# Kernel optimization log

Measured on AMD Instinct MI355X. Metric: run time of the kernel, lower is better.

The kernel has to match this reference:

```python
import jax, jax.numpy as jnp
import numpy as np

UNITS = 50257
CUTOFF = [2000, 10000, UNITS]   # cutoff + [units], as in __init__
D = 1024
FACTOR = 4
N_CLUST = len(CUTOFF) - 1       # 2 tail clusters
HEAD_OUT = CUTOFF[0] + N_CLUST  # 2002 = head classes + one logit per cluster


def _tail_dims():
    dims = []
    for i in range(N_CLUST):
        dim = D / FACTOR ** (i + 1)
        dims.append(max(1, round(dim / 8)) * 8)
    return dims  # [256, 64]


def setup_inputs() -> dict:
    key = jax.random.key(0)
    ks = jax.random.split(key, 16)
    B, T = 2, 1024
    x = jax.random.normal(ks[0], (B, T, D), jnp.float32)
    targets = jax.random.randint(ks[1], (B, T), 0, UNITS)
    inp = {
        'x': x,
        'targets': targets,
        # head: Dense(D -> HEAD_OUT), use_bias=False (glorot-ish scaling)
        'head_kernel': jax.random.normal(ks[2], (D, HEAD_OUT), jnp.float32) / np.float32(np.sqrt(D)),
    }
    for i, dim in enumerate(_tail_dims()):
        out = CUTOFF[i + 1] - CUTOFF[i]
        inp[f'proj_kernel_{i}'] = jax.random.normal(ks[3 + 4 * i], (D, dim), jnp.float32) / np.float32(np.sqrt(D))
        inp[f'proj_bias_{i}'] = jnp.zeros((dim,), jnp.float32)
        inp[f'scale_kernel_{i}'] = jax.random.normal(ks[4 + 4 * i], (dim, out), jnp.float32) / np.float32(np.sqrt(dim))
        inp[f'scale_bias_{i}'] = jnp.zeros((out,), jnp.float32)
    return inp


def reference(x, targets, head_kernel,
              proj_kernel_0, proj_bias_0, scale_kernel_0, scale_bias_0,
              proj_kernel_1, proj_bias_1, scale_kernel_1, scale_bias_1):
    # Head: root logits over [head classes | cluster logits]
    root_logits = jnp.einsum('btd,dh->bth', x, head_kernel)          # [B,T,HEAD_OUT]
    root_logprobs = jax.nn.log_softmax(root_logits, axis=-1)
    parts = [root_logprobs[..., :CUTOFF[0]]]                          # head class logprobs
    tails = [(proj_kernel_0, proj_bias_0, scale_kernel_0, scale_bias_0),
             (proj_kernel_1, proj_bias_1, scale_kernel_1, scale_bias_1)]
    for i, (pk, pb, sk, sb) in enumerate(tails):
        h = jnp.einsum('btd,dk->btk', x, pk) + pb                     # low-rank projection
        logits = jnp.einsum('btk,kv->btv', h, sk) + sb                # cluster vocab slice
        clust_lp = root_logprobs[..., CUTOFF[0] + i:CUTOFF[0] + i + 1]
        parts.append(jax.nn.log_softmax(logits, axis=-1) + clust_lp)  # P(w) = P(cluster)*P(w|cluster)
    logprobs = jnp.concatenate(parts, axis=-1)                        # [B,T,UNITS]
    return jnp.exp(logprobs)
```

## Files before the change

### kernel.cpp

```cpp
#include <hip/hip_runtime.h>
#include <cstdint>
#include <cstddef>

#define ROWS    2048
#define DIM     1024
#define VOCAB   50257
#define CUT0    2000
#define CUT1    10000
#define PROJ_LD 320
#define LGTC_LD 10016

typedef __attribute__((ext_vector_type(8))) _Float16 f16x8;
typedef __attribute__((ext_vector_type(4))) float    f32x4;

__device__ __forceinline__ void gload_lds16(const void* g, void* l) {
    __builtin_amdgcn_global_load_lds(
        (const __attribute__((address_space(1))) void*)g,
        (__attribute__((address_space(3))) void*)l, 16, 0, 0);
}

__device__ __forceinline__ int swz8(int i, int n) {
    return (i & 7) * (n >> 3) + (i >> 3);
}

__device__ __forceinline__ void transpose_tile(
    const float* __restrict__ src, _Float16* __restrict__ dst,
    int K, int N, int local, int ntiles, float* tile)
{
    const int t  = threadIdx.x;
    const int bn = local % ntiles, bk = local / ntiles;
    const int tx = t & 31, ty = t >> 5;
    const int n0 = bn * 32, k0 = bk * 32;
#pragma unroll
    for (int i = 0; i < 4; ++i) {
        int kk = ty + i * 8;
        int n  = n0 + tx;
        tile[kk * 33 + tx] = (n < N) ? src[(size_t)(k0 + kk) * N + n] : 0.f;
    }
    __syncthreads();
#pragma unroll
    for (int i = 0; i < 4; ++i) {
        int nn = ty + i * 8;
        int r  = n0 + nn;
        dst[(size_t)r * K + k0 + tx] = (_Float16)tile[tx * 33 + nn];
    }
}

__global__ __launch_bounds__(256)
void k1_convert(const float* __restrict__ x, const float* __restrict__ head,
                const float* __restrict__ pk0, const float* __restrict__ pk1,
                _Float16* __restrict__ A, _Float16* __restrict__ headT,
                _Float16* __restrict__ pkT, float* __restrict__ S)
{
    __shared__ float tile[32 * 33];
    const int bid = blockIdx.x, t = threadIdx.x;

    if (bid >= 4480) {
        int i = (bid - 4480) * 256 + t;
        ((float4*)S)[i] = make_float4(0.f, 0.f, 0.f, 0.f);
        return;
    }
    if (bid < 2048) {
        int fid = bid * 256 + t;
        float4 v = ((const float4*)x)[fid];
        union { _Float16 h[4]; ushort4 u; } cv;
        cv.h[0] = (_Float16)v.x; cv.h[1] = (_Float16)v.y;
        cv.h[2] = (_Float16)v.z; cv.h[3] = (_Float16)v.w;
        ((ushort4*)A)[fid] = cv.u;
        return;
    }
    if (bid < 4096)
        transpose_tile(head, headT, 1024, 2002, bid - 2048, 64, tile);
    else if (bid < 4352)
        transpose_tile(pk0, pkT, 1024, 256, bid - 4096, 8, tile);
    else
        transpose_tile(pk1, pkT + 256 * 1024, 1024, 64, bid - 4352, 4, tile);
}

template<int MODE, int BM>
__device__ __forceinline__ void gemm_body(
    _Float16* As, _Float16* Bs,
    const _Float16* __restrict__ A, int lda,
    const _Float16* __restrict__ B, int K,
    int bx, int by, int Nvalid,
    const float* __restrict__ bias,
    const float* __restrict__ pb0, const float* __restrict__ pb1,
    _Float16* __restrict__ lgtC, float* __restrict__ root2,
    float* __restrict__ S, float* __restrict__ outF,
    _Float16* __restrict__ h)
{
    const int t    = threadIdx.x;
    const int lane = t & 63;
    const int w    = t >> 6;
    const int wr   = w >> 1, wc = w & 1;
    const int q    = lane >> 4, cl = lane & 15;
    const int row0blk = by * BM;
    const int col0blk = bx * 128;
    constexpr int MR = BM / 32;

    f32x4 acc[MR][4];
#pragma unroll
    for (int m = 0; m < MR; ++m)
#pragma unroll
        for (int n = 0; n < 4; ++n)
            acc[m][n] = (f32x4){0.f, 0.f, 0.f, 0.f};

    for (int k0 = 0; k0 < K; k0 += 64) {
        __syncthreads();
#pragma unroll
        for (int iss = 0; iss < MR; ++iss) {
            int ci  = iss * 256 + w * 64 + lane;
            int row = ci >> 3;
            int ch  = (ci & 7) ^ (row & 7);
            gload_lds16(A + (size_t)(row0blk + row) * lda + k0 + ch * 8,
                        As + (size_t)(iss * 256 + w * 64) * 8);
        }
#pragma unroll
        for (int iss = 0; iss < 4; ++iss) {
            int ci  = iss * 256 + w * 64 + lane;
            int row = ci >> 3;
            int ch  = (ci & 7) ^ (row & 7);
            gload_lds16(B + (size_t)(col0blk + row) * K + k0 + ch * 8,
                        Bs + (size_t)(iss * 256 + w * 64) * 8);
        }
        __syncthreads();

#pragma unroll
        for (int kk = 0; kk < 2; ++kk) {
            f16x8 a[MR], b[4];
#pragma unroll
            for (int m = 0; m < MR; ++m) {
                int row = wr * (BM / 2) + m * 16 + cl;
                int ch  = (kk * 4 + q) ^ (row & 7);
                a[m] = *(const f16x8*)(As + row * 64 + ch * 8);
            }
#pragma unroll
            for (int n = 0; n < 4; ++n) {
                int row = wc * 64 + n * 16 + cl;
                int ch  = (kk * 4 + q) ^ (row & 7);
                b[n] = *(const f16x8*)(Bs + row * 64 + ch * 8);
            }
#pragma unroll
            for (int m = 0; m < MR; ++m)
#pragma unroll
                for (int n = 0; n < 4; ++n)
                    acc[m][n] = __builtin_amdgcn_mfma_f32_16x16x32_f16(
                        a[m], b[n], acc[m][n], 0, 0, 0);
        }
    }
    __syncthreads();

    if (MODE == 3) {
#pragma unroll
        for (int m = 0; m < MR; ++m)
#pragma unroll
            for (int n = 0; n < 4; ++n) {
                int colseg = col0blk + wc * 64 + n * 16 + cl;
                if (colseg < PROJ_LD) {
                    float bv = (colseg < 256) ? pb0[colseg] : pb1[colseg - 256];
#pragma unroll
                    for (int j = 0; j < 4; ++j) {
                        int rg = row0blk + wr * (BM / 2) + m * 16 + q * 4 + j;
                        h[(size_t)rg * PROJ_LD + colseg] =
                            (_Float16)(acc[m][n][j] + bv);
                    }
                }
            }
        return;
    }

    float bn4[4];
#pragma unroll
    for (int n = 0; n < 4; ++n) {
        int colseg = col0blk + wc * 64 + n * 16 + cl;
        bn4[n] = (MODE != 0 && colseg < Nvalid) ? bias[colseg] : 0.f;
    }

    if (MODE == 4) {
#pragma unroll
        for (int m = 0; m < MR; ++m)
#pragma unroll
            for (int j = 0; j < 4; ++j) {
                int rg = row0blk + wr * (BM / 2) + m * 16 + q * 4 + j;
                float4 S4 = ((const float4*)S)[rg];
                float scl = __expf(root2[rg * 2 + 1]) / (S4.z * S4.x);
                size_t rb = (size_t)rg * VOCAB + CUT1;
#pragma unroll
                for (int n = 0; n < 4; ++n) {
                    int c = col0blk + wc * 64 + n * 16 + cl;
                    if (c < Nvalid)
                        outF[rb + c] = __expf(acc[m][n][j] + bn4[n]) * scl;
                }
            }
        return;
    }

    float* sred = (float*)As;
#pragma unroll
    for (int m = 0; m < MR; ++m)
#pragma unroll
        for (int j = 0; j < 4; ++j) {
            int rloc = wr * (BM / 2) + m * 16 + q * 4 + j;
            int rg   = row0blk + rloc;
            float sm = 0.f;
#pragma unroll
            for (int n = 0; n < 4; ++n) {
                int c = col0blk + wc * 64 + n * 16 + cl;
                float v = acc[m][n][j] + bn4[n];
                bool ok = c < Nvalid;
                if (MODE == 0 && ok) {
                    if (c < CUT0)
                        lgtC[(size_t)rg * LGTC_LD + c] = (_Float16)v;
                    else
                        root2[rg * 2 + (c - CUT0)] = v;
                }
                if (MODE == 1 && ok)
                    lgtC[(size_t)rg * LGTC_LD + CUT0 + c] = (_Float16)v;
                sm += ok ? __expf(v) : 0.f;
            }
#pragma unroll
            for (int d = 1; d < 16; d <<= 1)
                sm += __shfl_xor(sm, d);
            if (cl == 0) sred[wc * BM + rloc] = sm;
        }
    __syncthreads();
    if (t < BM) {
        const int sidx = (MODE == 0) ? 0 : (MODE == 1 ? 1 : 2);
        atomicAdd(&S[(row0blk + t) * 4 + sidx], sred[t] + sred[BM + t]);
    }
}

__global__ __launch_bounds__(256)
void k2_projroot(const _Float16* __restrict__ A, const _Float16* __restrict__ pkT,
                 const _Float16* __restrict__ headT,
                 const float* __restrict__ sk0, const float* __restrict__ sk1,
                 const float* __restrict__ pb0, const float* __restrict__ pb1,
                 _Float16* __restrict__ h, _Float16* __restrict__ lgtC,
                 _Float16* __restrict__ sk0T, _Float16* __restrict__ sk1T,
                 float* __restrict__ root2, float* __restrict__ S)
{
    __shared__ _Float16 As[128 * 64];
    __shared__ _Float16 Bs[128 * 64];
    const int bid = blockIdx.x;
    if (bid < 512) {
        int i = swz8(bid, 512);
        gemm_body<0, 64>(As, Bs, A, DIM, headT, 1024, i % 16, i / 16, 2002,
                         nullptr, nullptr, nullptr, lgtC, root2, S, nullptr,
                         nullptr);
    } else if (bid < 560) {
        int i = swz8(bid - 512, 48);
        gemm_body<3, 128>(As, Bs, A, DIM, pkT, 1024, i % 3, i / 3, PROJ_LD,
                          nullptr, pb0, pb1, nullptr, nullptr, nullptr,
                          nullptr, h);
    } else if (bid < 2576) {
        transpose_tile(sk0, sk0T, 256, 8000, bid - 560, 252, (float*)As);
    } else {
        transpose_tile(sk1, sk1T, 64, 40257, bid - 2576, 1260, (float*)As);
    }
}

__global__ __launch_bounds__(256)
void k3_scales(const _Float16* __restrict__ h, const _Float16* __restrict__ sk0T,
               const _Float16* __restrict__ sk1T,
               const float* __restrict__ sb0, const float* __restrict__ sb1,
               _Float16* __restrict__ lgtC, float* __restrict__ S)
{
    __shared__ _Float16 As[128 * 64];
    __shared__ _Float16 Bs[128 * 64];
    const int bid = blockIdx.x;
    if (bid < 1008) {
        int i = swz8(bid, 1008);
        gemm_body<1, 128>(As, Bs, h, PROJ_LD, sk0T, 256, i % 63, i / 63, 8000,
                          sb0, nullptr, nullptr, lgtC, nullptr, S, nullptr,
                          nullptr);
    } else {
        int i = swz8(bid - 1008, 5040);
        gemm_body<2, 128>(As, Bs, h + 256, PROJ_LD, sk1T, 64, i % 315, i / 315,
                          40257, sb1, nullptr, nullptr, nullptr, nullptr, S,
                          nullptr, nullptr);
    }
}

__global__ __launch_bounds__(256)
void k4_megafin(const _Float16* __restrict__ h, const _Float16* __restrict__ sk1T,
                const float* __restrict__ sb1, const _Float16* __restrict__ lgtC,
                const float* __restrict__ root2, const float* __restrict__ S,
                float* __restrict__ outF)
{
    __shared__ _Float16 As[128 * 64];
    __shared__ _Float16 Bs[128 * 64];
    const int bid = blockIdx.x;
    if (bid < 5040) {
        int i = swz8(bid, 5040);
        gemm_body<4, 128>(As, Bs, h + 256, PROJ_LD, sk1T, 64, i % 315, i / 315,
                          40257, sb1, nullptr, nullptr, nullptr,
                          (float*)root2, (float*)S, outF, nullptr);
        return;
    }
    const int r = bid - 5040;
    float4 S4 = ((const float4*)S)[r];
    float inv_r = 1.f / S4.x;
    float sc0   = __expf(root2[r * 2 + 0]) / (S4.y * S4.x);
    const _Float16* lrow = lgtC + (size_t)r * LGTC_LD;
    float* orow = outF + (size_t)r * VOCAB;
    for (int i8 = threadIdx.x; i8 < LGTC_LD / 8; i8 += 256) {
        uint4 raw = *(const uint4*)(lrow + i8 * 8);
        union { uint32_t u; _Float16 hh[2]; } pp[4];
        pp[0].u = raw.x; pp[1].u = raw.y; pp[2].u = raw.z; pp[3].u = raw.w;
        int c0 = i8 * 8;
#pragma unroll
        for (int k = 0; k < 4; ++k)
#pragma unroll
            for (int j = 0; j < 2; ++j) {
                int c = c0 + k * 2 + j;
                if (c < CUT1) {
                    float sc = (c < CUT0) ? inv_r : sc0;
                    orow[c] = __expf((float)pp[k].hh[j]) * sc;
                }
            }
    }
}

extern "C" void kernel_launch(void* const* d_in, const int* in_sizes, int n_in,
                              void* d_out, int out_size, void* d_ws, size_t ws_size,
                              hipStream_t stream)
{
    (void)in_sizes; (void)n_in; (void)out_size; (void)ws_size;

    const float* x    = (const float*)d_in[0];
    const float* head = (const float*)d_in[2];
    const float* pk0  = (const float*)d_in[3];
    const float* pb0  = (const float*)d_in[4];
    const float* sk0  = (const float*)d_in[5];
    const float* sb0  = (const float*)d_in[6];
    const float* pk1  = (const float*)d_in[7];
    const float* pb1  = (const float*)d_in[8];
    const float* sk1  = (const float*)d_in[9];
    const float* sb1  = (const float*)d_in[10];

    float* out = (float*)d_out;
    char*  ws  = (char*)d_ws;

    _Float16* lgtC  = (_Float16*)(ws);
    _Float16* A     = (_Float16*)(ws + 41025536);
    _Float16* headT = (_Float16*)(ws + 45219840);
    _Float16* pkT   = (_Float16*)(ws + 49414144);
    _Float16* sk0T  = (_Float16*)(ws + 50200576);
    _Float16* sk1T  = (_Float16*)(ws + 54329344);
    _Float16* h     = (_Float16*)(ws + 59490304);
    float*    root2 = (float*)(ws + 60801024);
    float*    S     = (float*)(ws + 60817408);

    const dim3 blk(256);

    k1_convert<<<dim3(4488), blk, 0, stream>>>(x, head, pk0, pk1,
                                               A, headT, pkT, S);
    k2_projroot<<<dim3(5096), blk, 0, stream>>>(A, pkT, headT, sk0, sk1,
                                                pb0, pb1, h, lgtC, sk0T, sk1T,
                                                root2, S);
    k3_scales<<<dim3(6048), blk, 0, stream>>>(h, sk0T, sk1T, sb0, sb1, lgtC, S);
    k4_megafin<<<dim3(7088), blk, 0, stream>>>(h, sk1T, sb1, lgtC, root2, S, out);
}
```

Baseline: 266.6 us.

## Replace LDS-staged GEMM with direct-register MFMA for small-K tail scale GEMMs

```diff
diff --git a/kernel.cpp b/kernel.cpp
--- a/kernel.cpp
+++ b/kernel.cpp
@@ -83,11 +83,9 @@
     const _Float16* __restrict__ A, int lda,
     const _Float16* __restrict__ B, int K,
     int bx, int by, int Nvalid,
-    const float* __restrict__ bias,
     const float* __restrict__ pb0, const float* __restrict__ pb1,
     _Float16* __restrict__ lgtC, float* __restrict__ root2,
-    float* __restrict__ S, float* __restrict__ outF,
-    _Float16* __restrict__ h)
+    float* __restrict__ S, _Float16* __restrict__ h)
 {
     const int t    = threadIdx.x;
     const int lane = t & 63;
@@ -169,19 +167,100 @@
         return;
     }
 
+    float* sred = (float*)As;
+#pragma unroll
+    for (int m = 0; m < MR; ++m)
+#pragma unroll
+        for (int j = 0; j < 4; ++j) {
+            int rloc = wr * (BM / 2) + m * 16 + q * 4 + j;
+            int rg   = row0blk + rloc;
+            float sm = 0.f;
+#pragma unroll
+            for (int n = 0; n < 4; ++n) {
+                int c = col0blk + wc * 64 + n * 16 + cl;
+                float v = acc[m][n][j];
+                bool ok = c < Nvalid;
+                if (ok) {
+                    if (c < CUT0)
+                        lgtC[(size_t)rg * LGTC_LD + c] = (_Float16)v;
+                    else
+                        root2[rg * 2 + (c - CUT0)] = v;
+                }
+                sm += ok ? __expf(v) : 0.f;
+            }
+#pragma unroll
+            for (int d = 1; d < 16; d <<= 1)
+                sm += __shfl_xor(sm, d);
+            if (cl == 0) sred[wc * BM + rloc] = sm;
+        }
+    __syncthreads();
+    if (t < BM)
+        atomicAdd(&S[(row0blk + t) * 4 + 0], sred[t] + sred[BM + t]);
+}
+
+template<int MODE, int KK>
+__device__ __forceinline__ void gemm_direct(
+    const _Float16* __restrict__ A, int lda,
+    const _Float16* __restrict__ B,
+    int bx, int by, int Nvalid,
+    const float* __restrict__ bias,
+    _Float16* __restrict__ lgtC, const float* __restrict__ root2,
+    float* __restrict__ S, float* __restrict__ outF)
+{
+    __shared__ float sred[256];
+    const int t    = threadIdx.x;
+    const int lane = t & 63;
+    const int w    = t >> 6;
+    const int wr   = w >> 1, wc = w & 1;
+    const int q    = lane >> 4, cl = lane & 15;
+    const int row0blk = by * 128;
+    const int col0blk = bx * 128;
+
+    f32x4 acc[4][4];
+#pragma unroll
+    for (int m = 0; m < 4; ++m)
+#pragma unroll
+        for (int n = 0; n < 4; ++n)
+            acc[m][n] = (f32x4){0.f, 0.f, 0.f, 0.f};
+
+    const _Float16* ap[4];
+    const _Float16* bp[4];
+#pragma unroll
+    for (int m = 0; m < 4; ++m)
+        ap[m] = A + (size_t)(row0blk + wr * 64 + m * 16 + cl) * lda + q * 8;
+#pragma unroll
+    for (int n = 0; n < 4; ++n)
+        bp[n] = B + (size_t)(col0blk + wc * 64 + n * 16 + cl) * KK + q * 8;
+
+#pragma unroll
+    for (int ks = 0; ks < KK / 32; ++ks) {
+        const int ko = ks * 32;
+        f16x8 a[4], b[4];
+#pragma unroll
+        for (int m = 0; m < 4; ++m) a[m] = *(const f16x8*)(ap[m] + ko);
+#pragma unroll
+        for (int n = 0; n < 4; ++n) b[n] = *(const f16x8*)(bp[n] + ko);
+#pragma unroll
+        for (int m = 0; m < 4; ++m)
+#pragma unroll
+            for (int n = 0; n < 4; ++n)
+                acc[m][n] = __builtin_amdgcn_mfma_f32_16x16x32_f16(
+                    a[m], b[n], acc[m][n], 0, 0, 0);
+    }
+
     float bn4[4];
 #pragma unroll
     for (int n = 0; n < 4; ++n) {
         int colseg = col0blk + wc * 64 + n * 16 + cl;
-        bn4[n] = (MODE != 0 && colseg < Nvalid) ? bias[colseg] : 0.f;
+        bn4[n] = (colseg < Nvalid) ? bias[colseg] : 0.f;
     }
 
     if (MODE == 4) {
 #pragma unroll
-        for (int m = 0; m < MR; ++m)
+        for (int m = 0; m < 4; ++m)
 #pragma unroll
             for (int j = 0; j < 4; ++j) {
-                int rg = row0blk + wr * (BM / 2) + m * 16 + q * 4 + j;
+                int rg = row0blk + wr * 64 + m * 16 + q * 4 + j;
                 float4 S4 = ((const float4*)S)[rg];
                 float scl = __expf(root2[rg * 2 + 1]) / (S4.z * S4.x);
                 size_t rb = (size_t)rg * VOCAB + CUT1;
@@ -195,12 +274,11 @@
         return;
     }
 
-    float* sred = (float*)As;
-#pragma unroll
-    for (int m = 0; m < MR; ++m)
+#pragma unroll
+    for (int m = 0; m < 4; ++m)
 #pragma unroll
         for (int j = 0; j < 4; ++j) {
-            int rloc = wr * (BM / 2) + m * 16 + q * 4 + j;
+            int rloc = wr * 64 + m * 16 + q * 4 + j;
             int rg   = row0blk + rloc;
             float sm = 0.f;
 #pragma unroll
@@ -208,12 +286,6 @@
                 int c = col0blk + wc * 64 + n * 16 + cl;
                 float v = acc[m][n][j] + bn4[n];
                 bool ok = c < Nvalid;
-                if (MODE == 0 && ok) {
-                    if (c < CUT0)
-                        lgtC[(size_t)rg * LGTC_LD + c] = (_Float16)v;
-                    else
-                        root2[rg * 2 + (c - CUT0)] = v;
-                }
                 if (MODE == 1 && ok)
                     lgtC[(size_t)rg * LGTC_LD + CUT0 + c] = (_Float16)v;
                 sm += ok ? __expf(v) : 0.f;
@@ -221,12 +293,12 @@
 #pragma unroll
             for (int d = 1; d < 16; d <<= 1)
                 sm += __shfl_xor(sm, d);
-            if (cl == 0) sred[wc * BM + rloc] = sm;
+            if (cl == 0) sred[wc * 128 + rloc] = sm;
         }
     __syncthreads();
-    if (t < BM) {
-        const int sidx = (MODE == 0) ? 0 : (MODE == 1 ? 1 : 2);
-        atomicAdd(&S[(row0blk + t) * 4 + sidx], sred[t] + sred[BM + t]);
+    if (t < 128) {
+        const int sidx = (MODE == 1) ? 1 : 2;
+        atomicAdd(&S[(row0blk + t) * 4 + sidx], sred[t] + sred[128 + t]);
     }
 }
 
@@ -245,13 +317,11 @@
     if (bid < 512) {
         int i = swz8(bid, 512);
         gemm_body<0, 64>(As, Bs, A, DIM, headT, 1024, i % 16, i / 16, 2002,
-                         nullptr, nullptr, nullptr, lgtC, root2, S, nullptr,
-                         nullptr);
+                         nullptr, nullptr, lgtC, root2, S, nullptr);
     } else if (bid < 560) {
         int i = swz8(bid - 512, 48);
         gemm_body<3, 128>(As, Bs, A, DIM, pkT, 1024, i % 3, i / 3, PROJ_LD,
-                          nullptr, pb0, pb1, nullptr, nullptr, nullptr,
-                          nullptr, h);
+                          pb0, pb1, nullptr, nullptr, nullptr, h);
     } else if (bid < 2576) {
         transpose_tile(sk0, sk0T, 256, 8000, bid - 560, 252, (float*)As);
     } else {
@@ -265,19 +335,15 @@
                const float* __restrict__ sb0, const float* __restrict__ sb1,
                _Float16* __restrict__ lgtC, float* __restrict__ S)
 {
-    __shared__ _Float16 As[128 * 64];
-    __shared__ _Float16 Bs[128 * 64];
     const int bid = blockIdx.x;
     if (bid < 1008) {
         int i = swz8(bid, 1008);
-        gemm_body<1, 128>(As, Bs, h, PROJ_LD, sk0T, 256, i % 63, i / 63, 8000,
-                          sb0, nullptr, nullptr, lgtC, nullptr, S, nullptr,
-                          nullptr);
+        gemm_direct<1, 256>(h, PROJ_LD, sk0T, i % 63, i / 63, 8000,
+                            sb0, lgtC, nullptr, S, nullptr);
     } else {
         int i = swz8(bid - 1008, 5040);
-        gemm_body<2, 128>(As, Bs, h + 256, PROJ_LD, sk1T, 64, i % 315, i / 315,
-                          40257, sb1, nullptr, nullptr, nullptr, nullptr, S,
-                          nullptr, nullptr);
+        gemm_direct<2, 64>(h + 256, PROJ_LD, sk1T, i % 315, i / 315, 40257,
+                           sb1, nullptr, nullptr, S, nullptr);
     }
 }
 
@@ -287,14 +353,11 @@
                 const float* __restrict__ root2, const float* __restrict__ S,
                 float* __restrict__ outF)
 {
-    __shared__ _Float16 As[128 * 64];
-    __shared__ _Float16 Bs[128 * 64];
     const int bid = blockIdx.x;
     if (bid < 5040) {
         int i = swz8(bid, 5040);
-        gemm_body<4, 128>(As, Bs, h + 256, PROJ_LD, sk1T, 64, i % 315, i / 315,
-                          40257, sb1, nullptr, nullptr, nullptr,
-                          (float*)root2, (float*)S, outF, nullptr);
+        gemm_direct<4, 64>(h + 256, PROJ_LD, sk1T, i % 315, i / 315, 40257,
+                           sb1, nullptr, root2, (float*)S, outF);
         return;
     }
     const int r = bid - 5040;
```

After: 320.5 us. 20.2% more time.
